# Performance work log

Measured on AMD Instinct MI355X. Metric: run time of the kernel, lower is better.

The kernel has to match this reference:

```python
import jax, jax.numpy as jnp
import numpy as np

B, T, IN, H = 64, 512, 128, 512


def _lstm_layer(x, W_ih, W_hh, b_ih, b_hh):
    """Single unidirectional LSTM layer, batch_first input x: [B,T,in].
    PyTorch gate order: i, f, g, o. Returns outputs [B,T,H]."""
    # Precompute input contribution for all timesteps: [T,B,4H]
    xg = jnp.einsum('bti,gi->tbg', x, W_ih) + (b_ih + b_hh)
    Bt = x.shape[0]
    h0 = jnp.zeros((Bt, W_hh.shape[1]), x.dtype)
    c0 = jnp.zeros_like(h0)

    def step(carry, xt):
        h, c = carry
        g = xt + h @ W_hh.T  # [B,4H]
        i, f, gg, o = jnp.split(g, 4, axis=-1)
        i = jax.nn.sigmoid(i)
        f = jax.nn.sigmoid(f)
        gg = jnp.tanh(gg)
        o = jax.nn.sigmoid(o)
        c = f * c + i * gg
        h = o * jnp.tanh(c)
        return (h, c), h

    (_, _), hs = jax.lax.scan(step, (h0, c0), xg)
    return jnp.transpose(hs, (1, 0, 2))  # [B,T,H]


def setup_inputs() -> dict:
    key = jax.random.key(0)
    ks = jax.random.split(key, 11)
    s_in = 1.0 / np.sqrt(H)  # PyTorch LSTM init scale U(-1/sqrt(H), 1/sqrt(H))
    u = lambda k, shape: jax.random.uniform(k, shape, jnp.float32, -s_in, s_in)
    return {
        'x': jax.random.normal(ks[0], (B, T, IN), jnp.float32),
        'W_ih0': u(ks[1], (4 * H, IN)),
        'W_hh0': u(ks[2], (4 * H, H)),
        'b_ih0': u(ks[3], (4 * H,)),
        'b_hh0': u(ks[4], (4 * H,)),
        'W_ih1': u(ks[5], (4 * H, H)),
        'W_hh1': u(ks[6], (4 * H, H)),
        'b_ih1': u(ks[7], (4 * H,)),
        'b_hh1': u(ks[8], (4 * H,)),
        'W_fc': u(ks[9], (1, H)),
        'b_fc': u(ks[10], (1,)),
    }


def reference(x, W_ih0, W_hh0, b_ih0, b_hh0, W_ih1, W_hh1, b_ih1, b_hh1, W_fc, b_fc):
    out = _lstm_layer(x, W_ih0, W_hh0, b_ih0, b_hh0)
    out = _lstm_layer(out, W_ih1, W_hh1, b_ih1, b_hh1)
    logits = out[:, -1, :] @ W_fc.T + b_fc  # [B,1]
    return logits
```

## Files before the change

### kernel.cpp

```cpp
#include <hip/hip_runtime.h>


#define NWG 64
#define NB 64
#define NT 512
#define NH 512
#define BLK 512
#define SREC (NWG * BLK)
#define FPAD 16

typedef float f32x4 __attribute__((ext_vector_type(4)));
typedef __bf16 bf16x4 __attribute__((ext_vector_type(4)));
typedef __bf16 bf16x8 __attribute__((ext_vector_type(8)));
typedef unsigned long long u64;
typedef unsigned u32;

__device__ __forceinline__ bf16x4 ld8_bypass(const __bf16* p) {
    u64 v = __hip_atomic_load((const u64*)p, __ATOMIC_RELAXED, __HIP_MEMORY_SCOPE_AGENT);
    bf16x4 r; __builtin_memcpy(&r, &v, 8); return r;
}
__device__ __forceinline__ void st8_bypass(__bf16* p, u64 v) {
    __hip_atomic_store((u64*)p, v, __ATOMIC_RELAXED, __HIP_MEMORY_SCOPE_AGENT);
}

__device__ __forceinline__ void wait_flags(const unsigned* flags, unsigned target, int lane) {
    int g = 0;
    for (;;) {
        unsigned f = __hip_atomic_load((unsigned*)&flags[lane * FPAD],
                                       __ATOMIC_RELAXED, __HIP_MEMORY_SCOPE_AGENT);
        if (__all((int)(f >= target))) break;
        if (++g > (1 << 17)) break;
    }
}

__device__ __forceinline__ unsigned short bfbits(float f) {
    __bf16 h = (__bf16)f; unsigned short u; __builtin_memcpy(&u, &h, 2); return u;
}

__global__ void prep_kernel(unsigned short* hinit, unsigned short* hs1, unsigned* fl) {
    int i = blockIdx.x * blockDim.x + threadIdx.x;
    if (i < SREC) hinit[i] = 0;
    if (i < 2 * SREC) hs1[i] = 0;
    if (i < 2 * NWG * FPAD) fl[i] = 0;
}

template<int KIH, int IS_L0>
__device__ __forceinline__ void layer_body(
    char* Wl, float (*gbuf)[36], u32 (*hstage32)[4],
    int wg,
    const float* __restrict__ W_ih, const float* __restrict__ W_hh,
    const float* __restrict__ b_ih, const float* __restrict__ b_hh,
    const float* __restrict__ x_f32,
    __bf16* __restrict__ h0_all,
    const __bf16* __restrict__ hinit,
    __bf16* __restrict__ hbuf,
    float* __restrict__ h_final,
    unsigned* __restrict__ flags_self,
    const unsigned* __restrict__ flags_dep)
{
    constexpr int KTOT = KIH + NH;
    constexpr int NCH_A = KIH / 32;
    constexpr int NCH_B = NH / 32;
    constexpr int ROWB = KTOT * 2;

    const int tid = threadIdx.x;
    const int hcol0 = wg * 8;

    {
        constexpr int CPR = KTOT / 8;
        for (int cid = tid; cid < 32 * CPR; cid += 256) {
            const int r = cid / CPR;
            const int k0 = (cid - r * CPR) * 8;
            const int grow = (r >> 3) * NH + hcol0 + (r & 7);
            const float* src = (k0 < KIH) ? (W_ih + (size_t)grow * KIH + k0)
                                          : (W_hh + (size_t)grow * NH + (k0 - KIH));
            union { __bf16 h[8]; uint4 u; } tmp;
            #pragma unroll
            for (int j = 0; j < 8; ++j) tmp.h[j] = (__bf16)src[j];
            const unsigned off = (unsigned)(r * ROWB) +
                (((unsigned)(2 * k0)) ^ ((unsigned)((r & 7) << 4)));
            *(uint4*)(Wl + off) = tmp.u;
        }
    }

    const int eb = tid >> 2, ecp = (tid & 3) * 2;
    float bI[2], bF[2], bG[2], bO[2];
    #pragma unroll
    for (int j = 0; j < 2; ++j) {
        const int c = hcol0 + ecp + j;
        bI[j] = b_ih[c] + b_hh[c];
        bF[j] = b_ih[NH + c] + b_hh[NH + c];
        bG[j] = b_ih[2 * NH + c] + b_hh[2 * NH + c];
        bO[j] = b_ih[3 * NH + c] + b_hh[3 * NH + c];
    }
    float c0 = 0.f, c1 = 0.f;
    __syncthreads();

    const int lane = tid & 63;
    const int wid = tid >> 6;
    const int bt = wid * 16;
    const int arow = bt + (lane & 15);
    const int q4 = ((lane >> 4) & 3) * 4;
    const char* wrow0 = Wl + (lane & 15) * ROWB;
    const char* wrow1 = wrow0 + 16 * ROWB;
    const unsigned bsz = (unsigned)((lane & 7) << 4);
    const int aoff = arow * 8 + (q4 & 4);
    const int bsub = (q4 >> 3);

    auto wfragp = [&](const char* wr, int k0) -> bf16x8 {
        const bf16x4 lo = *(const bf16x4*)(wr + (((unsigned)(2 * (k0 + q4))) ^ bsz));
        const bf16x4 hi = *(const bf16x4*)(wr + (((unsigned)(2 * (k0 + 16 + q4))) ^ bsz));
        return __builtin_shufflevector(lo, hi, 0, 1, 2, 3, 4, 5, 6, 7);
    };
    auto mk8 = [&](bf16x4 lo, bf16x4 hi) -> bf16x8 {
        return __builtin_shufflevector(lo, hi, 0, 1, 2, 3, 4, 5, 6, 7);
    };

    for (int t = 0; t < NT; ++t) {
        const __bf16* __restrict__ hprev;
        __bf16* __restrict__ hout;
        if constexpr (IS_L0 != 0) {
            hprev = (t == 0) ? hinit : (h0_all + (size_t)(t - 1) * SREC);
            hout = h0_all + (size_t)t * SREC;
        } else {
            hprev = hbuf + (size_t)(t & 1) * SREC;
            hout = hbuf + (size_t)((t + 1) & 1) * SREC;
        }

        f32x4 p0a = {0,0,0,0}, p0b = {0,0,0,0};
        f32x4 p1a = {0,0,0,0}, p1b = {0,0,0,0};

        if constexpr (IS_L0 != 0) {
            const float* xb = x_f32 + ((size_t)arow * NT + t) * KIH;
            #pragma unroll
            for (int kk = 0; kk < NCH_A; ++kk) {
                const float4 lo = *(const float4*)(xb + kk * 32 + q4);
                const float4 hi = *(const float4*)(xb + kk * 32 + 16 + q4);
                const bf16x4 alo = {(__bf16)lo.x, (__bf16)lo.y, (__bf16)lo.z, (__bf16)lo.w};
                const bf16x4 ahi = {(__bf16)hi.x, (__bf16)hi.y, (__bf16)hi.z, (__bf16)hi.w};
                const bf16x8 av = mk8(alo, ahi);
                f32x4& d0 = (kk & 1) ? p0b : p0a;
                d0 = __builtin_amdgcn_mfma_f32_16x16x32_bf16(av, wfragp(wrow0, kk * 32), d0, 0, 0, 0);
                f32x4& d1 = (kk & 1) ? p1b : p1a;
                d1 = __builtin_amdgcn_mfma_f32_16x16x32_bf16(av, wfragp(wrow1, kk * 32), d1, 0, 0, 0);
            }
            if (t > 0 && wid == 0) wait_flags(flags_self, (unsigned)t, lane);
            __syncthreads();
        } else {
            if (wid == 0) wait_flags(flags_dep, (unsigned)(t + 1), lane);
            if (wid == 1 && t > 0) wait_flags(flags_self, (unsigned)t, lane);
            __syncthreads();
        }

        bf16x4 aBlo[NCH_B], aBhi[NCH_B];
        #pragma unroll
        for (int kk = 0; kk < NCH_B; ++kk) {
            const __bf16* base = hprev + (4 * kk + bsub) * BLK + aoff;
            aBlo[kk] = ld8_bypass(base);
            aBhi[kk] = ld8_bypass(base + 2 * BLK);
        }
        if constexpr (IS_L0 == 0) {
            const __bf16* hA = h0_all + (size_t)t * SREC;
            bf16x4 aAlo[NCH_A], aAhi[NCH_A];
            #pragma unroll
            for (int kk = 0; kk < NCH_A; ++kk) {
                const __bf16* base = hA + (4 * kk + bsub) * BLK + aoff;
                aAlo[kk] = ld8_bypass(base);
                aAhi[kk] = ld8_bypass(base + 2 * BLK);
            }
            #pragma unroll
            for (int kk = 0; kk < NCH_A; ++kk) {
                const bf16x8 av = mk8(aAlo[kk], aAhi[kk]);
                f32x4& d0 = (kk & 1) ? p0b : p0a;
                d0 = __builtin_amdgcn_mfma_f32_16x16x32_bf16(av, wfragp(wrow0, kk * 32), d0, 0, 0, 0);
                f32x4& d1 = (kk & 1) ? p1b : p1a;
                d1 = __builtin_amdgcn_mfma_f32_16x16x32_bf16(av, wfragp(wrow1, kk * 32), d1, 0, 0, 0);
            }
        }
        #pragma unroll
        for (int kk = 0; kk < NCH_B; ++kk) {
            const bf16x8 av = mk8(aBlo[kk], aBhi[kk]);
            f32x4& d0 = (kk & 1) ? p0b : p0a;
            d0 = __builtin_amdgcn_mfma_f32_16x16x32_bf16(av, wfragp(wrow0, KIH + kk * 32), d0, 0, 0, 0);
            f32x4& d1 = (kk & 1) ? p1b : p1a;
            d1 = __builtin_amdgcn_mfma_f32_16x16x32_bf16(av, wfragp(wrow1, KIH + kk * 32), d1, 0, 0, 0);
        }

        const f32x4 s0 = p0a + p0b, s1 = p1a + p1b;
        #pragma unroll
        for (int i = 0; i < 4; ++i) {
            gbuf[bt + ((lane >> 4) & 3) * 4 + i][lane & 15]        = s0[i];
            gbuf[bt + ((lane >> 4) & 3) * 4 + i][16 + (lane & 15)] = s1[i];
        }
        __syncthreads();

        {
            float hh[2]; float cc[2] = {c0, c1};
            #pragma unroll
            for (int j = 0; j < 2; ++j) {
                const int c = ecp + j;
                const float gi = gbuf[eb][c]      + bI[j];
                const float gf = gbuf[eb][8 + c]  + bF[j];
                const float gg = gbuf[eb][16 + c] + bG[j];
                const float go = gbuf[eb][24 + c] + bO[j];
                const float ii = 1.f / (1.f + __expf(-gi));
                const float ff = 1.f / (1.f + __expf(-gf));
                const float g2 = 2.f / (1.f + __expf(-2.f * gg)) - 1.f;
                const float oo = 1.f / (1.f + __expf(-go));
                const float cn = ff * cc[j] + ii * g2;
                const float th = 2.f / (1.f + __expf(-2.f * cn)) - 1.f;
                hh[j] = oo * th;
                cc[j] = cn;
            }
            c0 = cc[0]; c1 = cc[1];
            hstage32[eb][tid & 3] = (u32)bfbits(hh[0]) | ((u32)bfbits(hh[1]) << 16);
            if constexpr (IS_L0 == 0) {
                if (t == NT - 1) {
                    h_final[(size_t)eb * NH + hcol0 + ecp]     = hh[0];
                    h_final[(size_t)eb * NH + hcol0 + ecp + 1] = hh[1];
                }
            }
        }
        __syncthreads();

        if (tid < 128) {
            const u64 v = ((const u64*)hstage32)[tid];
            st8_bypass(hout + (size_t)wg * BLK + tid * 4, v);
        }
        asm volatile("s_waitcnt vmcnt(0)" ::: "memory");
        __syncthreads();
        if (tid == 0)
            __hip_atomic_store(&flags_self[wg * FPAD], (unsigned)(t + 1),
                               __ATOMIC_RELAXED, __HIP_MEMORY_SCOPE_AGENT);
    }
}

__launch_bounds__(256, 2)
__global__ void lstm_fused_kernel(
    const float* W_ih0, const float* W_hh0, const float* b_ih0, const float* b_hh0,
    const float* W_ih1, const float* W_hh1, const float* b_ih1, const float* b_hh1,
    const float* x, __bf16* h0_all, __bf16* hinit, __bf16* hs1,
    float* hfin, unsigned* fl0, unsigned* fl1)
{
    __shared__ __align__(16) char Wl[32 * 2048];
    __shared__ float gbuf[64][36];
    __shared__ u32 hstage32[64][4];

    if (blockIdx.x < NWG) {
        layer_body<128, 1>(Wl, gbuf, hstage32, blockIdx.x,
                           W_ih0, W_hh0, b_ih0, b_hh0,
                           x, h0_all, hinit, nullptr, nullptr, fl0, nullptr);
    } else {
        layer_body<512, 0>(Wl, gbuf, hstage32, blockIdx.x - NWG,
                           W_ih1, W_hh1, b_ih1, b_hh1,
                           nullptr, h0_all, hinit, hs1, hfin, fl1, fl0);
    }
}

__global__ void fc_kernel(const float* __restrict__ hfin,
                          const float* __restrict__ w_fc,
                          const float* __restrict__ b_fc,
                          float* __restrict__ out) {
    __shared__ float red[64][9];
    const int tid = threadIdx.x;
    const int b = tid >> 3, p = tid & 7;
    const int k0 = p * 64;
    float s = 0.f;
    #pragma unroll 8
    for (int k = 0; k < 64; ++k) s += hfin[(size_t)b * NH + k0 + k] * w_fc[k0 + k];
    red[b][p] = s;
    __syncthreads();
    if (p == 0) {
        float a = 0.f;
        #pragma unroll
        for (int j = 0; j < 8; ++j) a += red[b][j];
        out[b] = a + b_fc[0];
    }
}

extern "C" void kernel_launch(void* const* d_in, const int* in_sizes, int n_in,
                              void* d_out, int out_size, void* d_ws, size_t ws_size,
                              hipStream_t stream) {
    const float* x     = (const float*)d_in[0];
    const float* W_ih0 = (const float*)d_in[1];
    const float* W_hh0 = (const float*)d_in[2];
    const float* b_ih0 = (const float*)d_in[3];
    const float* b_hh0 = (const float*)d_in[4];
    const float* W_ih1 = (const float*)d_in[5];
    const float* W_hh1 = (const float*)d_in[6];
    const float* b_ih1 = (const float*)d_in[7];
    const float* b_hh1 = (const float*)d_in[8];
    const float* W_fc  = (const float*)d_in[9];
    const float* b_fc  = (const float*)d_in[10];

    char* ws = (char*)d_ws;
    __bf16*  h0_all = (__bf16*)(ws);
    __bf16*  hinit  = (__bf16*)(ws + 33554432);
    __bf16*  hs1    = (__bf16*)(ws + 33554432 + 65536);
    float*   hfin   = (float*) (ws + 33554432 + 196608);
    unsigned* fl0   = (unsigned*)(ws + 33554432 + 327680);
    unsigned* fl1   = fl0 + NWG * FPAD;

    prep_kernel<<<dim3(256), dim3(256), 0, stream>>>(
        (unsigned short*)hinit, (unsigned short*)hs1, fl0);

    lstm_fused_kernel<<<dim3(2 * NWG), dim3(256), 0, stream>>>(
        W_ih0, W_hh0, b_ih0, b_hh0, W_ih1, W_hh1, b_ih1, b_hh1,
        x, h0_all, hinit, hs1, hfin, fl0, fl1);

    fc_kernel<<<dim3(1), dim3(512), 0, stream>>>(hfin, W_fc, b_fc, (float*)d_out);
}
```

Baseline: 3.123 ms.

## Add coherence probe enabling cached h loads, prefetch layer-0 inputs, spread blocks across XCDs

Launches 512 blocks and keeps only two of every eight, so layer-0 and layer-1 workgroups sit at fixed residues of the block index. The intent appears to be pinning each layer to one XCD so hidden-state exchange can stay in a shared L2. A runtime probe checks that plain cached loads see peer writes; if they do, the recurrent h loads and stores drop the bypassing atomics. Layer 1 also prefetches the next step's layer-0 output after signalling, and its two flag waits are merged into one loop. This relies on an undocumented block-to-XCD mapping and a handshake-based probe, which adds startup cost and risks stale reads if the assumption fails.

```diff
diff --git a/kernel.cpp b/kernel.cpp
--- a/kernel.cpp
+++ b/kernel.cpp
@@ -15,48 +15,117 @@
 typedef unsigned long long u64;
 typedef unsigned u32;
 
-__device__ __forceinline__ bf16x4 ld8_bypass(const __bf16* p) {
-    u64 v = __hip_atomic_load((const u64*)p, __ATOMIC_RELAXED, __HIP_MEMORY_SCOPE_AGENT);
-    bf16x4 r; __builtin_memcpy(&r, &v, 8); return r;
-}
-__device__ __forceinline__ void st8_bypass(__bf16* p, u64 v) {
+__device__ __forceinline__ u64 ld8a(const __bf16* p) {
+    return __hip_atomic_load((const u64*)p, __ATOMIC_RELAXED, __HIP_MEMORY_SCOPE_AGENT);
+}
+__device__ __forceinline__ void st8a(__bf16* p, u64 v) {
     __hip_atomic_store((u64*)p, v, __ATOMIC_RELAXED, __HIP_MEMORY_SCOPE_AGENT);
 }
-
-__device__ __forceinline__ void wait_flags(const unsigned* flags, unsigned target, int lane) {
+__device__ __forceinline__ u32 ldfa(const u32* p) {
+    return __hip_atomic_load(p, __ATOMIC_RELAXED, __HIP_MEMORY_SCOPE_AGENT);
+}
+__device__ __forceinline__ void stfa(u32* p, u32 v) {
+    __hip_atomic_store(p, v, __ATOMIC_RELAXED, __HIP_MEMORY_SCOPE_AGENT);
+}
+__device__ __forceinline__ u64 ld8p(const __bf16* p) { return *(const u64*)p; }
+__device__ __forceinline__ void st8p(__bf16* p, u64 v) { *(u64*)p = v; }
+
+__device__ __forceinline__ unsigned short bfbits(float f) {
+    __bf16 h = (__bf16)f; unsigned short u; __builtin_memcpy(&u, &h, 2); return u;
+}
+
+__device__ __forceinline__ void wait_one(const u32* f, u32 ta, int lane) {
     int g = 0;
     for (;;) {
-        unsigned f = __hip_atomic_load((unsigned*)&flags[lane * FPAD],
-                                       __ATOMIC_RELAXED, __HIP_MEMORY_SCOPE_AGENT);
-        if (__all((int)(f >= target))) break;
+        u32 a = ldfa(&f[lane * FPAD]);
+        if (__all((int)(a >= ta))) break;
         if (++g > (1 << 17)) break;
     }
 }
-
-__device__ __forceinline__ unsigned short bfbits(float f) {
-    __bf16 h = (__bf16)f; unsigned short u; __builtin_memcpy(&u, &h, 2); return u;
-}
-
-__global__ void prep_kernel(unsigned short* hinit, unsigned short* hs1, unsigned* fl) {
+__device__ __forceinline__ void wait_two(const u32* fA, u32 ta, const u32* fB, u32 tb, int lane) {
+    int g = 0;
+    for (;;) {
+        u32 a = ldfa(&fA[lane * FPAD]);
+        u32 b = ldfa(&fB[lane * FPAD]);
+        if (__all((int)(a >= ta && b >= tb))) break;
+        if (++g > (1 << 17)) break;
+    }
+}
+
+#define CT_FLA0   0
+#define CT_FLA1   1024
+#define CT_FLB    2048
+#define CT_NONCE  3072
+#define CT_PRF    3104
+#define CT_VOTE   5152
+#define CT_PBUF   7200
+#define CT_N      9248
+
+__global__ void prep_kernel(unsigned short* hinit, unsigned short* hpar, u32* ctrl) {
     int i = blockIdx.x * blockDim.x + threadIdx.x;
     if (i < SREC) hinit[i] = 0;
-    if (i < 2 * SREC) hs1[i] = 0;
-    if (i < 2 * NWG * FPAD) fl[i] = 0;
-}
-
-template<int KIH, int IS_L0>
-__device__ __forceinline__ void layer_body(
-    char* Wl, float (*gbuf)[36], u32 (*hstage32)[4],
-    int wg,
+    if (hpar != nullptr && i < 2 * SREC) hpar[i] = 0;
+    for (int k = i; k < CT_N; k += gridDim.x * blockDim.x) ctrl[k] = 0;
+}
+
+__device__ bool run_probe(int layer, int wg, int tid, u32* ctrl, int allowFast) {
+    __shared__ int verd;
+    if (!allowFast) { if (tid == 0) verd = 0; __syncthreads(); return false; }
+    const int gwg = layer * NWG + wg;
+    if (tid == 0) {
+        if (wg == 0) {
+            u32 n = ((u32)clock64()) | 1u;
+            stfa(&ctrl[CT_NONCE + layer * FPAD], n);
+        }
+        u32 nonce = 0; int g = 0;
+        while ((nonce = ldfa(&ctrl[CT_NONCE + layer * FPAD])) == 0u)
+            { if (++g > (1 << 12)) break; }
+        u32 ok = 0;
+        if (nonce != 0u) {
+            ctrl[CT_PBUF + gwg * FPAD] = nonce ^ ((u32)wg * 2654435761u);
+            asm volatile("s_waitcnt vmcnt(0)" ::: "memory");
+            stfa(&ctrl[CT_PRF + gwg * FPAD], nonce);
+            const int p = (wg + 1) & (NWG - 1);
+            const int gp = layer * NWG + p;
+            u32 f = 0; g = 0;
+            while ((f = ldfa(&ctrl[CT_PRF + gp * FPAD])) != nonce)
+                { if (++g > (1 << 13)) break; }
+            if (f == nonce) {
+                asm volatile("" ::: "memory");
+                u32 got = ctrl[CT_PBUF + gp * FPAD];
+                asm volatile("" ::: "memory");
+                ok = (got == (nonce ^ ((u32)p * 2654435761u))) ? 1u : 0u;
+            }
+        }
+        stfa(&ctrl[CT_VOTE + gwg * FPAD], ok ? 1u : 2u);
+    }
+    int fastv = 0;
+    if (tid < 64) {
+        u32 v = 2u; int g = 0;
+        for (;;) {
+            v = ldfa(&ctrl[CT_VOTE + (layer * NWG + tid) * FPAD]);
+            if (__all((int)(v != 0u))) break;
+            if (++g > (1 << 14)) { v = 2u; break; }
+        }
+        fastv = __all((int)(v == 1u)) ? 1 : 0;
+        if (tid == 0) verd = fastv;
+    }
+    __syncthreads();
+    return verd != 0;
+}
+
+template<int KIH, int IS_L0, bool FAST, bool STEPIDX>
+__device__ void layer_loop(
+    char* Wl, float (*gbuf)[36], u32 (*hstage32)[4], int wg,
     const float* __restrict__ W_ih, const float* __restrict__ W_hh,
     const float* __restrict__ b_ih, const float* __restrict__ b_hh,
     const float* __restrict__ x_f32,
-    __bf16* __restrict__ h0_all,
+    const __bf16* __restrict__ hrec_dep,
+    __bf16* __restrict__ hself,
     const __bf16* __restrict__ hinit,
-    __bf16* __restrict__ hbuf,
     float* __restrict__ h_final,
-    unsigned* __restrict__ flags_self,
-    const unsigned* __restrict__ flags_dep)
+    u32* __restrict__ flA_self,
+    u32* __restrict__ flB)
 {
     constexpr int KTOT = KIH + NH;
     constexpr int NCH_A = KIH / 32;
@@ -112,19 +181,32 @@
         const bf16x4 hi = *(const bf16x4*)(wr + (((unsigned)(2 * (k0 + 16 + q4))) ^ bsz));
         return __builtin_shufflevector(lo, hi, 0, 1, 2, 3, 4, 5, 6, 7);
     };
-    auto mk8 = [&](bf16x4 lo, bf16x4 hi) -> bf16x8 {
+    auto mk8 = [&](u64 a, u64 b) -> bf16x8 {
+        bf16x4 lo, hi; __builtin_memcpy(&lo, &a, 8); __builtin_memcpy(&hi, &b, 8);
         return __builtin_shufflevector(lo, hi, 0, 1, 2, 3, 4, 5, 6, 7);
     };
 
+    u64 ra[2 * NCH_A];
+    if constexpr (IS_L0 == 0) {
+        if (wid == 0) wait_one(flB, 1u, lane);
+        __syncthreads();
+        #pragma unroll
+        for (int kk = 0; kk < NCH_A; ++kk) {
+            const __bf16* base = hrec_dep + (4 * kk + bsub) * BLK + aoff;
+            ra[2 * kk]     = ld8a(base);
+            ra[2 * kk + 1] = ld8a(base + 2 * BLK);
+        }
+    }
+
     for (int t = 0; t < NT; ++t) {
-        const __bf16* __restrict__ hprev;
-        __bf16* __restrict__ hout;
-        if constexpr (IS_L0 != 0) {
-            hprev = (t == 0) ? hinit : (h0_all + (size_t)(t - 1) * SREC);
-            hout = h0_all + (size_t)t * SREC;
+        const __bf16* hprev;
+        __bf16* hout;
+        if constexpr (STEPIDX) {
+            hprev = (t == 0) ? hinit : (hself + (size_t)(t - 1) * SREC);
+            hout = hself + (size_t)t * SREC;
         } else {
-            hprev = hbuf + (size_t)(t & 1) * SREC;
-            hout = hbuf + (size_t)((t + 1) & 1) * SREC;
+            hprev = hself + (size_t)(t & 1) * SREC;
+            hout = hself + (size_t)((t + 1) & 1) * SREC;
         }
 
         f32x4 p0a = {0,0,0,0}, p0b = {0,0,0,0};
@@ -138,39 +220,33 @@
                 const float4 hi = *(const float4*)(xb + kk * 32 + 16 + q4);
                 const bf16x4 alo = {(__bf16)lo.x, (__bf16)lo.y, (__bf16)lo.z, (__bf16)lo.w};
                 const bf16x4 ahi = {(__bf16)hi.x, (__bf16)hi.y, (__bf16)hi.z, (__bf16)hi.w};
-                const bf16x8 av = mk8(alo, ahi);
+                const bf16x8 av = __builtin_shufflevector(alo, ahi, 0, 1, 2, 3, 4, 5, 6, 7);
                 f32x4& d0 = (kk & 1) ? p0b : p0a;
                 d0 = __builtin_amdgcn_mfma_f32_16x16x32_bf16(av, wfragp(wrow0, kk * 32), d0, 0, 0, 0);
                 f32x4& d1 = (kk & 1) ? p1b : p1a;
                 d1 = __builtin_amdgcn_mfma_f32_16x16x32_bf16(av, wfragp(wrow1, kk * 32), d1, 0, 0, 0);
             }
-            if (t > 0 && wid == 0) wait_flags(flags_self, (unsigned)t, lane);
+            if (t > 0 && wid == 0) wait_one(flA_self, (u32)t, lane);
             __syncthreads();
         } else {
-            if (wid == 0) wait_flags(flags_dep, (unsigned)(t + 1), lane);
-            if (wid == 1 && t > 0) wait_flags(flags_self, (unsigned)t, lane);
+            if (wid == 0) {
+                const u32 tb = (t <= NT - 2) ? (u32)(t + 2) : 0u;
+                wait_two(flA_self, (t > 0) ? (u32)t : 0u, flB, tb, lane);
+            }
             __syncthreads();
         }
 
-        bf16x4 aBlo[NCH_B], aBhi[NCH_B];
+        u64 rb[2 * NCH_B];
         #pragma unroll
         for (int kk = 0; kk < NCH_B; ++kk) {
             const __bf16* base = hprev + (4 * kk + bsub) * BLK + aoff;
-            aBlo[kk] = ld8_bypass(base);
-            aBhi[kk] = ld8_bypass(base + 2 * BLK);
+            if constexpr (FAST) { rb[2*kk] = ld8p(base); rb[2*kk+1] = ld8p(base + 2*BLK); }
+            else                { rb[2*kk] = ld8a(base); rb[2*kk+1] = ld8a(base + 2*BLK); }
         }
         if constexpr (IS_L0 == 0) {
-            const __bf16* hA = h0_all + (size_t)t * SREC;
-            bf16x4 aAlo[NCH_A], aAhi[NCH_A];
             #pragma unroll
             for (int kk = 0; kk < NCH_A; ++kk) {
-                const __bf16* base = hA + (4 * kk + bsub) * BLK + aoff;
-                aAlo[kk] = ld8_bypass(base);
-                aAhi[kk] = ld8_bypass(base + 2 * BLK);
-            }
-            #pragma unroll
-            for (int kk = 0; kk < NCH_A; ++kk) {
-                const bf16x8 av = mk8(aAlo[kk], aAhi[kk]);
+                const bf16x8 av = mk8(ra[2 * kk], ra[2 * kk + 1]);
                 f32x4& d0 = (kk & 1) ? p0b : p0a;
                 d0 = __builtin_amdgcn_mfma_f32_16x16x32_bf16(av, wfragp(wrow0, kk * 32), d0, 0, 0, 0);
                 f32x4& d1 = (kk & 1) ? p1b : p1a;
@@ -179,7 +255,7 @@
         }
         #pragma unroll
         for (int kk = 0; kk < NCH_B; ++kk) {
-            const bf16x8 av = mk8(aBlo[kk], aBhi[kk]);
+            const bf16x8 av = mk8(rb[2 * kk], rb[2 * kk + 1]);
             f32x4& d0 = (kk & 1) ? p0b : p0a;
             d0 = __builtin_amdgcn_mfma_f32_16x16x32_bf16(av, wfragp(wrow0, KIH + kk * 32), d0, 0, 0, 0);
             f32x4& d1 = (kk & 1) ? p1b : p1a;
@@ -225,35 +301,79 @@
 
         if (tid < 128) {
             const u64 v = ((const u64*)hstage32)[tid];
-            st8_bypass(hout + (size_t)wg * BLK + tid * 4, v);
-        }
+            __bf16* dst = hout + (size_t)wg * BLK + (size_t)tid * 4;
+            if constexpr (FAST) {
+                st8p(dst, v);
+                if constexpr (IS_L0 != 0) st8a(dst, v);
+            } else {
+                st8a(dst, v);
+            }
+        }
+        if constexpr (FAST && IS_L0 != 0) asm volatile("s_waitcnt vmcnt(1)" ::: "memory");
+        else                              asm volatile("s_waitcnt vmcnt(0)" ::: "memory");
+        __syncthreads();
+        if (tid == 0) {
+            stfa(&flA_self[wg * FPAD], (u32)(t + 1));
+            if constexpr (IS_L0 != 0)
+                stfa(&flB[wg * FPAD], FAST ? (u32)t : (u32)(t + 1));
+        }
+        if constexpr (IS_L0 == 0) {
+            if (t < NT - 1) {
+                const __bf16* hA = hrec_dep + (size_t)(t + 1) * SREC;
+                #pragma unroll
+                for (int kk = 0; kk < NCH_A; ++kk) {
+                    const __bf16* base = hA + (4 * kk + bsub) * BLK + aoff;
+                    ra[2 * kk]     = ld8a(base);
+                    ra[2 * kk + 1] = ld8a(base + 2 * BLK);
+                }
+            }
+        }
+    }
+
+    if constexpr (IS_L0 != 0) {
         asm volatile("s_waitcnt vmcnt(0)" ::: "memory");
         __syncthreads();
-        if (tid == 0)
-            __hip_atomic_store(&flags_self[wg * FPAD], (unsigned)(t + 1),
-                               __ATOMIC_RELAXED, __HIP_MEMORY_SCOPE_AGENT);
+        if (tid == 0) stfa(&flB[wg * FPAD], (u32)NT);
     }
 }
 
 __launch_bounds__(256, 2)
-__global__ void lstm_fused_kernel(
+__global__ void lstm_kernel(
     const float* W_ih0, const float* W_hh0, const float* b_ih0, const float* b_hh0,
     const float* W_ih1, const float* W_hh1, const float* b_ih1, const float* b_hh1,
-    const float* x, __bf16* h0_all, __bf16* hinit, __bf16* hs1,
-    float* hfin, unsigned* fl0, unsigned* fl1)
+    const float* x, __bf16* hrec0, __bf16* h1buf, const __bf16* hinit, float* hfin,
+    u32* ctrl, int allowFastL0, int allowFastL1, int stepIdxL1)
 {
     __shared__ __align__(16) char Wl[32 * 2048];
     __shared__ float gbuf[64][36];
     __shared__ u32 hstage32[64][4];
 
-    if (blockIdx.x < NWG) {
-        layer_body<128, 1>(Wl, gbuf, hstage32, blockIdx.x,
-                           W_ih0, W_hh0, b_ih0, b_hh0,
-                           x, h0_all, hinit, nullptr, nullptr, fl0, nullptr);
+    const int res = blockIdx.x & 7;
+    if (res > 1) return;
+    const int wg = (int)(blockIdx.x >> 3);
+    const int tid = threadIdx.x;
+
+    u32* flA0 = ctrl + CT_FLA0;
+    u32* flA1 = ctrl + CT_FLA1;
+    u32* flB  = ctrl + CT_FLB;
+
+    if (res == 0) {
+        const bool f = run_probe(0, wg, tid, ctrl, allowFastL0);
+        if (f) layer_loop<128, 1, true,  true>(Wl, gbuf, hstage32, wg,
+                   W_ih0, W_hh0, b_ih0, b_hh0, x, nullptr, hrec0, hinit, nullptr, flA0, flB);
+        else   layer_loop<128, 1, false, true>(Wl, gbuf, hstage32, wg,
+                   W_ih0, W_hh0, b_ih0, b_hh0, x, nullptr, hrec0, hinit, nullptr, flA0, flB);
     } else {
-        layer_body<512, 0>(Wl, gbuf, hstage32, blockIdx.x - NWG,
-                           W_ih1, W_hh1, b_ih1, b_hh1,
-                           nullptr, h0_all, hinit, hs1, hfin, fl1, fl0);
+        const bool f = run_probe(1, wg, tid, ctrl, allowFastL1);
+        if (stepIdxL1 != 0) {
+            if (f) layer_loop<512, 0, true,  true>(Wl, gbuf, hstage32, wg,
+                       W_ih1, W_hh1, b_ih1, b_hh1, nullptr, hrec0, h1buf, hinit, hfin, flA1, flB);
+            else   layer_loop<512, 0, false, true>(Wl, gbuf, hstage32, wg,
+                       W_ih1, W_hh1, b_ih1, b_hh1, nullptr, hrec0, h1buf, hinit, hfin, flA1, flB);
+        } else {
+            layer_loop<512, 0, false, false>(Wl, gbuf, hstage32, wg,
+                       W_ih1, W_hh1, b_ih1, b_hh1, nullptr, hrec0, h1buf, hinit, hfin, flA1, flB);
+        }
     }
 }
 
@@ -294,19 +414,33 @@
     const float* b_fc  = (const float*)d_in[10];
 
     char* ws = (char*)d_ws;
-    __bf16*  h0_all = (__bf16*)(ws);
-    __bf16*  hinit  = (__bf16*)(ws + 33554432);
-    __bf16*  hs1    = (__bf16*)(ws + 33554432 + 65536);
-    float*   hfin   = (float*) (ws + 33554432 + 196608);
-    unsigned* fl0   = (unsigned*)(ws + 33554432 + 327680);
-    unsigned* fl1   = fl0 + NWG * FPAD;
+    size_t off = 0;
+    auto take = [&](size_t bytes) { char* p = ws + off; off += (bytes + 255) & ~(size_t)255; return p; };
+
+    __bf16* hrec0 = (__bf16*)take((size_t)NT * SREC * 2);
+    __bf16* hinit = (__bf16*)take(SREC * 2);
+    float*  hfin  = (float*) take(NB * NH * 4);
+    u32*    ctrl  = (u32*)   take(CT_N * 4);
+    const size_t base = off;
+    const size_t need_big = base + (size_t)NT * SREC * 2;
+
+    const bool big = (ws_size >= need_big);
+    __bf16* h1buf;
+    unsigned short* hpar_for_prep = nullptr;
+    if (big) {
+        h1buf = (__bf16*)take((size_t)NT * SREC * 2);
+    } else {
+        h1buf = (__bf16*)take((size_t)2 * SREC * 2);
+        hpar_for_prep = (unsigned short*)h1buf;
+    }
 
     prep_kernel<<<dim3(256), dim3(256), 0, stream>>>(
-        (unsigned short*)hinit, (unsigned short*)hs1, fl0);
-
-    lstm_fused_kernel<<<dim3(2 * NWG), dim3(256), 0, stream>>>(
+        (unsigned short*)hinit, hpar_for_prep, ctrl);
+
+    lstm_kernel<<<dim3(512), dim3(256), 0, stream>>>(
         W_ih0, W_hh0, b_ih0, b_hh0, W_ih1, W_hh1, b_ih1, b_hh1,
-        x, h0_all, hinit, hs1, hfin, fl0, fl1);
+        x, hrec0, h1buf, hinit, hfin, ctrl,
+        1, big ? 1 : 0, big ? 1 : 0);
 
     fc_kernel<<<dim3(1), dim3(512), 0, stream>>>(hfin, W_fc, b_fc, (float*)d_out);
 }
```

Measured after the change: 3.979 ms. 1.27x slower.
